# Performance work log

Hardware: AMD Instinct MI355X
Metric: run time of the kernel (lower is better)

Reference implementation:

```python
import jax, jax.numpy as jnp
import numpy as np
from jax import lax

FEAT = 56  # features_size
SR = 2     # sr_ratio
NUM_HEADS = 8

# Constant relative-distance indices, shape (N, N, 2) with values in [0, 2*FEAT-2]
_idx = np.array([[i, j] for i in range(FEAT) for j in range(FEAT)])
REL = jnp.asarray(_idx[None, :, :] - _idx[:, None, :] + FEAT - 1)  # (N, N, 2)


def setup_inputs() -> dict:
    key = jax.random.key(0)
    ks = jax.random.split(key, 8)
    dim = 256
    B = 4
    x = jax.random.normal(ks[0], (B, dim, FEAT, FEAT), dtype=jnp.float32)
    Wq = jax.random.normal(ks[1], (dim, dim), dtype=jnp.float32) * 0.02
    Wkv = jax.random.normal(ks[2], (dim, 2 * dim), dtype=jnp.float32) * 0.02
    sr_w = jax.random.normal(ks[3], (dim, dim, SR, SR), dtype=jnp.float32) * 0.02  # OIHW
    sr_b = jnp.zeros((dim,), dtype=jnp.float32)
    ln_g = jnp.ones((dim,), dtype=jnp.float32)
    ln_b = jnp.zeros((dim,), dtype=jnp.float32)
    pos_emb = jax.random.normal(ks[4], (2 * FEAT - 1, 2 * FEAT - 1), dtype=jnp.float32) * 0.2
    proj_w = jax.random.normal(ks[5], (dim, dim), dtype=jnp.float32) * 0.02
    proj_b = jnp.zeros((dim,), dtype=jnp.float32)
    return {"x": x, "Wq": Wq, "Wkv": Wkv, "sr_w": sr_w, "sr_b": sr_b,
            "ln_g": ln_g, "ln_b": ln_b, "pos_emb": pos_emb,
            "proj_w": proj_w, "proj_b": proj_b}


def reference(x, Wq, Wkv, sr_w, sr_b, ln_g, ln_b, pos_emb, proj_w, proj_b):
    B, C, H, W = x.shape
    N = H * W
    h = NUM_HEADS
    hd = C // h
    scale = hd ** -0.5

    x_q = x.reshape(B, C, N).transpose(0, 2, 1)            # (B, N, C)
    q = (x_q @ Wq).reshape(B, N, h, hd).transpose(0, 2, 1, 3)  # (B, h, N, hd)

    # spatial reduction conv (kernel=stride=SR) + layernorm
    xr = lax.conv_general_dilated(x, sr_w, (SR, SR), 'VALID',
                                  dimension_numbers=('NCHW', 'OIHW', 'NCHW'))
    xr = xr + sr_b[None, :, None, None]
    Nk = (H // SR) * (W // SR)
    x_kv = xr.reshape(B, C, Nk).transpose(0, 2, 1)          # (B, Nk, C)
    mu = jnp.mean(x_kv, axis=-1, keepdims=True)
    var = jnp.var(x_kv, axis=-1, keepdims=True)
    x_kv = (x_kv - mu) * lax.rsqrt(var + 1e-5) * ln_g + ln_b

    # kv projection; einops '(dim h l)' split: head_dim slowest, l fastest
    kv = (x_kv @ Wkv).reshape(B, Nk, hd, h, 2)
    k = kv[..., 0].transpose(0, 3, 1, 2)                    # (B, h, Nk, hd)
    v = kv[..., 1].transpose(0, 3, 1, 2)                    # (B, h, Nk, hd)

    attn = jnp.einsum('bhnd,bhmd->bhnm', q, k) * scale      # (B, h, N, Nk)
    bias = pos_emb[REL[..., 0], REL[..., 1]][:, :Nk]        # (N, Nk)
    attn = jax.nn.softmax(attn + bias, axis=-1)

    out = jnp.einsum('bhnm,bhmd->bhnd', attn, v)            # (B, h, N, hd)
    out = out.transpose(0, 2, 1, 3).reshape(B, N, C)
    out = out @ proj_w + proj_b
    return out.transpose(0, 2, 1).reshape(B, C, H, W)
```

## Files before the change

### kernel.cpp

```cpp
#include <hip/hip_runtime.h>
#include <hip/hip_bf16.h>

typedef float f32x4 __attribute__((ext_vector_type(4)));
typedef short s16x8 __attribute__((ext_vector_type(8)));
typedef unsigned short u16x4 __attribute__((ext_vector_type(4)));
typedef unsigned short u16x8 __attribute__((ext_vector_type(8)));

#define MFMA16(a,b,c) __builtin_amdgcn_mfma_f32_16x16x32_bf16(a,b,c,0,0,0)

#define NTOK 3136
#define NKV  784
#define NKVP 800
#define CD   256
#define NH   8
#define HD   32
#define PEW  111
#define LOG2E 1.4426950408889634f
#define SC2  (0.17677669529663687f * 1.4426950408889634f)

static __device__ __forceinline__ unsigned short f2b(float f){
  unsigned int u = __float_as_uint(f);
  return (unsigned short)((u + 0x7fffu + ((u>>16)&1u)) >> 16);
}
static __device__ __forceinline__ float b2f(unsigned short u){
  return __uint_as_float(((unsigned int)u)<<16);
}
static __device__ __forceinline__ void gload16(const unsigned short* g, unsigned short* l){
  __builtin_amdgcn_global_load_lds(
      (const __attribute__((address_space(1))) unsigned int*)g,
      (__attribute__((address_space(3))) unsigned int*)l, 16, 0, 0);
}
static __device__ __forceinline__ s16x8 pack8(const float* p){
  union { uint4 u; s16x8 s; } w;
  unsigned int a0=__float_as_uint(p[0])+0x8000u, a1=__float_as_uint(p[1])+0x8000u;
  unsigned int a2=__float_as_uint(p[2])+0x8000u, a3=__float_as_uint(p[3])+0x8000u;
  unsigned int a4=__float_as_uint(p[4])+0x8000u, a5=__float_as_uint(p[5])+0x8000u;
  unsigned int a6=__float_as_uint(p[6])+0x8000u, a7=__float_as_uint(p[7])+0x8000u;
  w.u.x = (a0>>16) | (a1 & 0xFFFF0000u);
  w.u.y = (a2>>16) | (a3 & 0xFFFF0000u);
  w.u.z = (a4>>16) | (a5 & 0xFFFF0000u);
  w.u.w = (a6>>16) | (a7 & 0xFFFF0000u);
  return w.s;
}

__global__ __launch_bounds__(256) void k_prep(
      const float* __restrict__ Wq, const float* __restrict__ Wkv,
      const float* __restrict__ pw, const float* __restrict__ srw,
      const float* __restrict__ pos, const float* __restrict__ x,
      unsigned short* __restrict__ WqT, unsigned short* __restrict__ WkvT,
      unsigned short* __restrict__ pwT, unsigned short* __restrict__ srwb2,
      unsigned short* __restrict__ bias2, unsigned short* __restrict__ xbf,
      unsigned short* __restrict__ kb, unsigned short* __restrict__ vT){
  __shared__ float tile[64][65];
  const int blk = blockIdx.x, t = threadIdx.x;
  const int tx = t&15, ty = t>>4;
  if (blk < 64){
    const float* src; unsigned short* dst; int sr0, sc0, sstr;
    if (blk < 16){ src=Wq; dst=WqT; sstr=256; sr0=(blk>>2)*64; sc0=(blk&3)*64; }
    else if (blk < 32){ int b2=blk-16; src=pw; dst=pwT; sstr=256; sr0=(b2>>2)*64; sc0=(b2&3)*64; }
    else { int b2=blk-32; src=Wkv; dst=WkvT; sstr=512; sr0=(b2>>3)*64; sc0=(b2&7)*64; }
#pragma unroll
    for (int j=0;j<4;++j){
      f32x4 v = *(const f32x4*)&src[(size_t)(sr0+ty+j*16)*sstr + sc0 + tx*4];
      tile[ty+j*16][tx*4+0]=v[0]; tile[ty+j*16][tx*4+1]=v[1];
      tile[ty+j*16][tx*4+2]=v[2]; tile[ty+j*16][tx*4+3]=v[3];
    }
    __syncthreads();
    const int nr = t>>2, ccb = (t&3)*16;
    u16x8 o0, o1;
#pragma unroll
    for (int u=0;u<8;++u){ o0[u]=f2b(tile[ccb+u][nr]); o1[u]=f2b(tile[ccb+8+u][nr]); }
    unsigned short* dp = &dst[(size_t)(sc0+nr)*256 + sr0 + ccb];
    *(u16x8*)dp = o0;
    *(u16x8*)(dp+8) = o1;
  } else if (blk < 1088){
    int j = (blk-64)*256 + t;
    int o=j>>10, rem=j&1023, khw=rem>>8, ci=rem&255;
    srwb2[j] = f2b(srw[o*1024 + ci*4 + khw]);
  } else if (blk < 1216){
    int i = (blk-1088)*256 + t;
    if (i < 16384){
      int bh=i>>9, r=i&511, ridx=r>>5, d=r&31;
      int row = 776 + (ridx&7) + (ridx>>3)*16;
      kb[((size_t)bh*NKVP + row)*HD + d] = 0;
    } else {
      int j=i-16384;
      int bh=j>>9, r=j&511, d=r>>4, key=784+(r&15);
      vT[((size_t)bh*HD + d)*NKVP + key] = 0;
    }
  } else if (blk < 4352){
    int n = blk - 1216;
    if (t < 200){
      int nr2 = (n*9363)>>19, nc = n - nr2*56;
      u16x4 o;
#pragma unroll
      for (int j=0;j<4;++j){
        int key = t*4 + j;
        float v;
        if (key < NKV){
          int tt = (key*9363)>>19, mm = key - tt*56;
          v = pos[(tt-nr2+55)*PEW + (mm-nc+55)] * LOG2E;
        } else v = -100000.f;
        o[j] = f2b(v);
      }
      *(u16x4*)&bias2[(size_t)n*NKVP + t*4] = o;
    }
  } else {
    int bx = blk - 4352;
    const int n0 = (bx%49)*64; int c4 = bx/49;
    const int c0 = (c4&3)*64, b = c4>>2;
#pragma unroll
    for (int j=0;j<4;++j){
      f32x4 v = *(const f32x4*)&x[(size_t)(b*CD + c0+ty+j*16)*NTOK + n0 + tx*4];
      tile[ty+j*16][tx*4+0]=v[0]; tile[ty+j*16][tx*4+1]=v[1];
      tile[ty+j*16][tx*4+2]=v[2]; tile[ty+j*16][tx*4+3]=v[3];
    }
    __syncthreads();
    const int nr = t>>2, ccb = (t&3)*16;
    u16x8 o0, o1;
#pragma unroll
    for (int u=0;u<8;++u){ o0[u]=f2b(tile[ccb+u][nr]); o1[u]=f2b(tile[ccb+8+u][nr]); }
    unsigned short* dst = &xbf[((size_t)b*NTOK + n0+nr)*CD + c0 + ccb];
    *(u16x8*)dst = o0;
    *(u16x8*)(dst+8) = o1;
  }
}

__global__ __launch_bounds__(256) void k_qc(const unsigned short* __restrict__ xbf,
      const unsigned short* __restrict__ WqT, const unsigned short* __restrict__ srwb2,
      const float* __restrict__ srb, unsigned short* __restrict__ qb,
      float* __restrict__ convo){
  const int gid = blockIdx.x;
  const int tid=threadIdx.x, wv=tid>>6, l=tid&63, g=l>>4, ln16=l&15;
  if (gid < 784){
    const int bx = gid % 196, by = gid / 196;
    const int bI = bx/49;
    const int n0 = (bx%49)*64;
    const int m0 = n0 + (wv>>1)*32;
    const int c0 = by*64 + (wv&1)*32;
    const unsigned short* ap0 = &xbf[((size_t)bI*NTOK + m0+ln16)*CD + g*8];
    const unsigned short* ap1 = ap0 + 16*CD;
    const unsigned short* bp0 = &WqT[(size_t)(c0+ln16)*CD + g*8];
    const unsigned short* bp1 = bp0 + 16*CD;
    f32x4 acc[2][2] = {};
    s16x8 a0 = *(const s16x8*)ap0, a1 = *(const s16x8*)ap1;
    s16x8 w0 = *(const s16x8*)bp0, w1 = *(const s16x8*)bp1;
#pragma unroll
    for (int k0=0; k0<CD; k0+=32){
      s16x8 na0 = *(const s16x8*)(ap0 + k0+32);
      s16x8 na1 = *(const s16x8*)(ap1 + k0+32);
      s16x8 nw0 = *(const s16x8*)(bp0 + k0+32);
      s16x8 nw1 = *(const s16x8*)(bp1 + k0+32);
      acc[0][0] = MFMA16(a0, w0, acc[0][0]);
      acc[0][1] = MFMA16(a0, w1, acc[0][1]);
      acc[1][0] = MFMA16(a1, w0, acc[1][0]);
      acc[1][1] = MFMA16(a1, w1, acc[1][1]);
      a0=na0; a1=na1; w0=nw0; w1=nw1;
    }
#pragma unroll
    for (int mi=0;mi<2;++mi)
#pragma unroll
      for (int ni=0;ni<2;++ni){
        int c = c0 + ni*16 + ln16;
#pragma unroll
        for (int r=0;r<4;++r){
          int n = m0 + mi*16 + g*4 + r;
          qb[((size_t)bI*NTOK + n)*CD + c] = f2b(acc[mi][ni][r] * SC2);
        }
      }
  } else {
    const int cid = gid - 784;
    const int m0 = (cid%49)*64 + (wv>>1)*32;
    const int c0 = (cid/49)*64 + (wv&1)*32;
    size_t abase[2][4];
#pragma unroll
    for (int mi=0;mi<2;++mi){
      int m = m0 + mi*16 + ln16;
      int bb = (m>=2352)?3:(m>=1568)?2:(m>=784)?1:0;
      int nk = m - bb*784;
      int pp = (nk*9363)>>18, qq = nk - pp*28;
#pragma unroll
      for (int khw=0;khw<4;++khw){
        int kh = khw>>1, kw = khw&1;
        abase[mi][khw] = ((size_t)bb*NTOK + (2*pp+kh)*56 + 2*qq+kw)*CD;
      }
    }
    const unsigned short* wp0 = &srwb2[(size_t)(c0+ln16)*1024 + g*8];
    const unsigned short* wp1 = wp0 + 16*1024;
    f32x4 acc[2][2] = {};
    s16x8 a0 = *(const s16x8*)&xbf[abase[0][0] + g*8];
    s16x8 a1 = *(const s16x8*)&xbf[abase[1][0] + g*8];
    s16x8 w0 = *(const s16x8*)wp0;
    s16x8 w1 = *(const s16x8*)wp1;
#pragma unroll
    for (int s=0; s<32; ++s){
      const int s1 = s+1;
      const int khw2 = (s1>>3)&3, kc2 = (s1&7)*32;
      const int woff = (s1&31)*32;
      s16x8 na0 = *(const s16x8*)&xbf[abase[0][khw2] + kc2 + g*8];
      s16x8 na1 = *(const s16x8*)&xbf[abase[1][khw2] + kc2 + g*8];
      s16x8 nw0 = *(const s16x8*)(wp0 + woff);
      s16x8 nw1 = *(const s16x8*)(wp1 + woff);
      acc[0][0] = MFMA16(a0, w0, acc[0][0]);
      acc[0][1] = MFMA16(a0, w1, acc[0][1]);
      acc[1][0] = MFMA16(a1, w0, acc[1][0]);
      acc[1][1] = MFMA16(a1, w1, acc[1][1]);
      a0=na0; a1=na1; w0=nw0; w1=nw1;
    }
#pragma unroll
    for (int mi=0;mi<2;++mi)
#pragma unroll
      for (int ni=0;ni<2;++ni){
        int c = c0 + ni*16 + ln16;
        float bias = srb[c];
#pragma unroll
        for (int r=0;r<4;++r){
          int m = m0 + mi*16 + g*4 + r;
          convo[(size_t)m*CD + c] = acc[mi][ni][r] + bias;
        }
      }
  }
}

__global__ __launch_bounds__(256) void k_kvln(const float* __restrict__ co,
      const float* __restrict__ gam, const float* __restrict__ bet,
      const unsigned short* __restrict__ WkvT, unsigned short* __restrict__ kb,
      unsigned short* __restrict__ vT){
  __shared__ unsigned short As[64*256];
  const int tid=threadIdx.x, wv=tid>>6, l=tid&63, g=l>>4, ln16=l&15;
  const int m0blk = blockIdx.x*64;
  {
    const int rl = tid>>2, cs = (tid&3)*64;
    const float* src = &co[(size_t)(m0blk+rl)*CD + cs];
    f32x4 vals[16];
    float s=0.f, s2=0.f;
#pragma unroll
    for (int i=0;i<16;++i){
      vals[i] = *(const f32x4*)(src + i*4);
#pragma unroll
      for (int q=0;q<4;++q){ s += vals[i][q]; s2 += vals[i][q]*vals[i][q]; }
    }
    s += __shfl_xor(s,1); s2 += __shfl_xor(s2,1);
    s += __shfl_xor(s,2); s2 += __shfl_xor(s2,2);
    float mu = s*(1.f/CD);
    float rs = rsqrtf(s2*(1.f/CD) - mu*mu + 1e-5f);
#pragma unroll
    for (int u=0;u<8;++u){
      f32x4 g4a = *(const f32x4*)&gam[cs+u*8];
      f32x4 g4b = *(const f32x4*)&gam[cs+u*8+4];
      f32x4 b4a = *(const f32x4*)&bet[cs+u*8];
      f32x4 b4b = *(const f32x4*)&bet[cs+u*8+4];
      u16x8 o;
#pragma unroll
      for (int q=0;q<4;++q){
        o[q]   = f2b((vals[u*2][q]  -mu)*rs*g4a[q] + b4a[q]);
        o[4+q] = f2b((vals[u*2+1][q]-mu)*rs*g4b[q] + b4b[q]);
      }
      int off = (rl*256 + cs + u*8) ^ ((rl&7)<<3);
      *(u16x8*)&As[off] = o;
    }
  }
  __syncthreads();
  const int mw0 = (wv>>1)*32;
  const int c0 = blockIdx.y*64 + (wv&1)*32;
  const unsigned short* bp0 = &WkvT[(size_t)(c0+ln16)*CD + g*8];
  const unsigned short* bp1 = bp0 + 16*CD;
  f32x4 acc[2][2] = {};
  s16x8 w0 = *(const s16x8*)bp0, w1 = *(const s16x8*)bp1;
  const int mr0 = mw0 + ln16, mr1 = mw0 + 16 + ln16;
#pragma unroll
  for (int k0=0; k0<CD; k0+=32){
    s16x8 a0 = *(const s16x8*)&As[(mr0*256 + k0 + g*8) ^ ((mr0&7)<<3)];
    s16x8 a1 = *(const s16x8*)&As[(mr1*256 + k0 + g*8) ^ ((mr1&7)<<3)];
    s16x8 nw0 = w0, nw1 = w1;
    if (k0 < CD-32){
      nw0 = *(const s16x8*)(bp0 + k0+32);
      nw1 = *(const s16x8*)(bp1 + k0+32);
    }
    acc[0][0] = MFMA16(a0, w0, acc[0][0]);
    acc[0][1] = MFMA16(a0, w1, acc[0][1]);
    acc[1][0] = MFMA16(a1, w0, acc[1][0]);
    acc[1][1] = MFMA16(a1, w1, acc[1][1]);
    w0=nw0; w1=nw1;
  }
#pragma unroll
  for (int mi=0;mi<2;++mi)
#pragma unroll
    for (int ni=0;ni<2;++ni){
      int c2 = c0 + ni*16 + ln16;
      int d = c2>>4, hh = (c2>>1)&7;
#pragma unroll
      for (int r=0;r<4;++r){
        int m = m0blk + mw0 + mi*16 + g*4 + r;
        int bq = (m>=2352)?3:(m>=1568)?2:(m>=784)?1:0;
        int nk = m - bq*784;
        unsigned short val = f2b(acc[mi][ni][r]);
        if (c2&1){
          vT[(((size_t)bq*NH+hh)*HD + d)*NKVP + nk] = val;
        } else {
          int chunk = nk & ~31, pos = nk & 31;
          int gg = pos>>3, jj = pos&7;
          int row = (jj<4) ? (gg*4+jj) : (16 + gg*4 + (jj-4));
          kb[(((size_t)bq*NH+hh)*NKVP + chunk + row)*HD + d] = val;
        }
      }
    }
}

__global__ __launch_bounds__(256) void k_attn(const unsigned short* __restrict__ qb,
      const unsigned short* __restrict__ kb, const unsigned short* __restrict__ vT,
      const unsigned short* __restrict__ bias2, unsigned short* __restrict__ aout){
  __shared__ unsigned short kv0[2048], kv1[2048], kv2[2048];
  const int tid=threadIdx.x, wv=tid>>6, l=tid&63, g=l>>4, ln16=l&15;
  const int bh = blockIdx.x, b = bh>>3, h = bh&7;
  const int nq0 = blockIdx.y*128 + wv*16;
  const int nq1 = nq0 + 64;
  const bool act1 = (nq1 < NTOK);
  const int nq1c = act1 ? nq1 : nq0;
  const s16x8 qf0 = *(const s16x8*)&qb[((size_t)b*NTOK + nq0  + ln16)*CD + h*HD + g*8];
  const s16x8 qf1 = *(const s16x8*)&qb[((size_t)b*NTOK + nq1c + ln16)*CD + h*HD + g*8];
  const unsigned short* kbase = kb + (size_t)bh*NKVP*HD;
  const unsigned short* vbase = vT + (size_t)bh*HD*NKVP;
  const unsigned short* bp0 = bias2 + (size_t)(nq0  + ln16)*NKVP + g*8;
  const unsigned short* bp1 = bias2 + (size_t)(nq1c + ln16)*NKVP + g*8;
  const int lslot = ((l&3)^((l>>3)&3))*8;
  const unsigned short* sp = (wv < 2)
      ? (kbase + (size_t)(wv*16 + (l>>2))*HD + lslot)
      : (vbase + (size_t)((wv-2)*16 + (l>>2))*NKVP + lslot);
  const int sstep = (wv < 2) ? 1024 : 32;
  const int ko0 = ln16*32 + (g ^ ((ln16>>1)&3))*8;
  unsigned short *bA = kv0, *bB = kv1, *bC = kv2;
  f32x4 acc00={}, acc01={}, acc10={}, acc11={};
  float S0=0.f, S1=0.f;
  const f32x4 zf = {};
  gload16(sp, bA + wv*512);
  u16x8 bb0 = *(const u16x8*)bp0;
  u16x8 bb1 = *(const u16x8*)bp1;
  gload16(sp + sstep, bB + wv*512);
  u16x8 c0v = *(const u16x8*)(bp0 + 32);
  u16x8 c1v = *(const u16x8*)(bp1 + 32);
  for (int it=0; it<25; ++it){
    if (it < 23) asm volatile("s_waitcnt vmcnt(3)" ::: "memory");
    else         asm volatile("s_waitcnt vmcnt(0)" ::: "memory");
    __builtin_amdgcn_s_barrier();
    __builtin_amdgcn_sched_barrier(0);
    u16x8 n0v = c0v, n1v = c1v;
    if (it < 23){
      gload16(sp + (it+2)*sstep, bC + wv*512);
      n0v = *(const u16x8*)(bp0 + (it+2)*32);
      n1v = *(const u16x8*)(bp1 + (it+2)*32);
    }
    s16x8 ka0 = *(const s16x8*)&bA[ko0];
    s16x8 ka1 = *(const s16x8*)&bA[512 + ko0];
    s16x8 v0  = *(const s16x8*)&bA[1024 + ko0];
    s16x8 v1  = *(const s16x8*)&bA[1536 + ko0];
    __builtin_amdgcn_s_setprio(1);
    f32x4 d00 = MFMA16(ka0, qf0, zf);
    f32x4 d10 = MFMA16(ka1, qf0, zf);
    f32x4 d01 = MFMA16(ka0, qf1, zf);
    f32x4 d11 = MFMA16(ka1, qf1, zf);
    float p0[8], p1[8];
#pragma unroll
    for (int r=0;r<4;++r){
      p0[r]   = exp2f(d00[r] + b2f(bb0[r]));
      p0[4+r] = exp2f(d10[r] + b2f(bb0[4+r]));
      p1[r]   = exp2f(d01[r] + b2f(bb1[r]));
      p1[4+r] = exp2f(d11[r] + b2f(bb1[4+r]));
    }
    S0 += ((p0[0]+p0[1])+(p0[2]+p0[3])) + ((p0[4]+p0[5])+(p0[6]+p0[7]));
    S1 += ((p1[0]+p1[1])+(p1[2]+p1[3])) + ((p1[4]+p1[5])+(p1[6]+p1[7]));
    s16x8 pf0 = pack8(p0);
    s16x8 pf1 = pack8(p1);
    acc00 = MFMA16(pf0, v0, acc00);
    acc01 = MFMA16(pf0, v1, acc01);
    acc10 = MFMA16(pf1, v0, acc10);
    acc11 = MFMA16(pf1, v1, acc11);
    __builtin_amdgcn_s_setprio(0);
    unsigned short* tmp = bA; bA = bB; bB = bC; bC = tmp;
    bb0 = c0v; c0v = n0v;
    bb1 = c1v; c1v = n1v;
  }
  S0 += __shfl_xor(S0, 16); S0 += __shfl_xor(S0, 32);
  S1 += __shfl_xor(S1, 16); S1 += __shfl_xor(S1, 32);
#pragma unroll
  for (int r=0;r<4;++r){
    float inv = 1.f / __shfl(S0, g*4 + r);
    int n = nq0 + g*4 + r;
    aout[((size_t)b*NTOK + n)*CD + h*HD + ln16]      = f2b(acc00[r]*inv);
    aout[((size_t)b*NTOK + n)*CD + h*HD + 16 + ln16] = f2b(acc01[r]*inv);
  }
  if (act1){
#pragma unroll
    for (int r=0;r<4;++r){
      float inv = 1.f / __shfl(S1, g*4 + r);
      int n = nq1 + g*4 + r;
      aout[((size_t)b*NTOK + n)*CD + h*HD + ln16]      = f2b(acc10[r]*inv);
      aout[((size_t)b*NTOK + n)*CD + h*HD + 16 + ln16] = f2b(acc11[r]*inv);
    }
  }
}

__global__ __launch_bounds__(256) void k_proj(const unsigned short* __restrict__ ain,
      const unsigned short* __restrict__ pwT, const float* __restrict__ pb,
      float* __restrict__ out){
  const int tid=threadIdx.x, wv=tid>>6, l=tid&63, g=l>>4, ln16=l&15;
  const int bI = blockIdx.x/49;
  const int n0 = (blockIdx.x%49)*64;
  const int nsub = n0 + (wv&1)*32;
  const int c0 = blockIdx.y*64 + (wv>>1)*32;
  const unsigned short* ap0 = &pwT[(size_t)(c0+ln16)*CD + g*8];
  const unsigned short* ap1 = ap0 + 16*CD;
  const unsigned short* bp0 = &ain[((size_t)bI*NTOK + nsub+ln16)*CD + g*8];
  const unsigned short* bp1 = bp0 + 16*CD;
  f32x4 acc[2][2] = {};
  s16x8 a0 = *(const s16x8*)ap0, a1 = *(const s16x8*)ap1;
  s16x8 w0 = *(const s16x8*)bp0, w1 = *(const s16x8*)bp1;
#pragma unroll
  for (int k0=0; k0<CD; k0+=32){
    s16x8 na0 = *(const s16x8*)(ap0 + k0+32);
    s16x8 na1 = *(const s16x8*)(ap1 + k0+32);
    s16x8 nw0 = *(const s16x8*)(bp0 + k0+32);
    s16x8 nw1 = *(const s16x8*)(bp1 + k0+32);
    acc[0][0] = MFMA16(a0, w0, acc[0][0]);
    acc[0][1] = MFMA16(a0, w1, acc[0][1]);
    acc[1][0] = MFMA16(a1, w0, acc[1][0]);
    acc[1][1] = MFMA16(a1, w1, acc[1][1]);
    a0=na0; a1=na1; w0=nw0; w1=nw1;
  }
#pragma unroll
  for (int mi=0;mi<2;++mi)
#pragma unroll
    for (int r=0;r<4;++r){
      int c = c0 + mi*16 + g*4 + r;
      float bias = pb[c];
#pragma unroll
      for (int ni=0;ni<2;++ni){
        int n = nsub + ni*16 + ln16;
        out[((size_t)bI*CD + c)*NTOK + n] = acc[mi][ni][r] + bias;
      }
    }
}

extern "C" void kernel_launch(void* const* d_in, const int* in_sizes, int n_in,
                              void* d_out, int out_size, void* d_ws, size_t ws_size,
                              hipStream_t stream){
  const float* x   = (const float*)d_in[0];
  const float* Wq  = (const float*)d_in[1];
  const float* Wkv = (const float*)d_in[2];
  const float* srw = (const float*)d_in[3];
  const float* srb = (const float*)d_in[4];
  const float* lng = (const float*)d_in[5];
  const float* lnb = (const float*)d_in[6];
  const float* pos = (const float*)d_in[7];
  const float* pw  = (const float*)d_in[8];
  const float* pb  = (const float*)d_in[9];
  float* out = (float*)d_out;

  unsigned char* p = (unsigned char*)d_ws;
  unsigned short* WqT   = (unsigned short*)(p + 0);
  unsigned short* WkvT  = (unsigned short*)(p + 131072);
  unsigned short* pwT   = (unsigned short*)(p + 393216);
  unsigned short* srwb2 = (unsigned short*)(p + 524288);
  unsigned short* bias2 = (unsigned short*)(p + 1048576);
  unsigned short* xbf   = (unsigned short*)(p + 6066176);
  unsigned short* qbuf  = (unsigned short*)(p + 12488704);
  float*          convo = (float*)        (p + 18911232);
  unsigned short* kbuf  = (unsigned short*)(p + 22122496);
  unsigned short* vT    = (unsigned short*)(p + 23760896);
  unsigned short* aout  = (unsigned short*)(p + 25399296);

  k_prep <<<5136, 256, 0, stream>>>(Wq, Wkv, pw, srw, pos, x,
                                    WqT, WkvT, pwT, srwb2, bias2, xbf, kbuf, vT);
  k_qc   <<<980, 256, 0, stream>>>(xbf, WqT, srwb2, srb, qbuf, convo);
  k_kvln <<<dim3(49,8), 256, 0, stream>>>(convo, lng, lnb, WkvT, kbuf, vT);
  k_attn <<<dim3(32,25), 256, 0, stream>>>(qbuf, kbuf, vT, bias2, aout);
  k_proj <<<dim3(196,4), 256, 0, stream>>>(aout, pwT, pb, out);
}
```

Measured before the change: 200.1 us.

## Deepen GEMM prefetch to two stages and make attention waves independent

The GEMM-style kernels (q, conv, kv, proj) now prefetch operands two k-steps ahead through a three-slot register ring instead of one step ahead. The attention kernel is restructured so each wave owns 16 query rows and its own double-buffered LDS K/V tiles, with no block-wide barriers. The grid doubles from 25 to 49 row blocks to compensate for half the rows per block. This removes barrier stalls and the shared loading split between waves. In exchange, each wave loads its own K/V, so global and LDS traffic rise and register pressure from the deeper prefetch grows.

```diff
diff --git a/kernel.cpp b/kernel.cpp
--- a/kernel.cpp
+++ b/kernel.cpp
@@ -143,19 +143,24 @@
     const unsigned short* bp0 = &WqT[(size_t)(c0+ln16)*CD + g*8];
     const unsigned short* bp1 = bp0 + 16*CD;
     f32x4 acc[2][2] = {};
-    s16x8 a0 = *(const s16x8*)ap0, a1 = *(const s16x8*)ap1;
-    s16x8 w0 = *(const s16x8*)bp0, w1 = *(const s16x8*)bp1;
-#pragma unroll
-    for (int k0=0; k0<CD; k0+=32){
-      s16x8 na0 = *(const s16x8*)(ap0 + k0+32);
-      s16x8 na1 = *(const s16x8*)(ap1 + k0+32);
-      s16x8 nw0 = *(const s16x8*)(bp0 + k0+32);
-      s16x8 nw1 = *(const s16x8*)(bp1 + k0+32);
-      acc[0][0] = MFMA16(a0, w0, acc[0][0]);
-      acc[0][1] = MFMA16(a0, w1, acc[0][1]);
-      acc[1][0] = MFMA16(a1, w0, acc[1][0]);
-      acc[1][1] = MFMA16(a1, w1, acc[1][1]);
-      a0=na0; a1=na1; w0=nw0; w1=nw1;
+    s16x8 ra0[3], ra1[3], rw0[3], rw1[3];
+    ra0[0]=*(const s16x8*)ap0; ra1[0]=*(const s16x8*)ap1;
+    rw0[0]=*(const s16x8*)bp0; rw1[0]=*(const s16x8*)bp1;
+    ra0[1]=*(const s16x8*)(ap0+32); ra1[1]=*(const s16x8*)(ap1+32);
+    rw0[1]=*(const s16x8*)(bp0+32); rw1[1]=*(const s16x8*)(bp1+32);
+#pragma unroll
+    for (int i=0;i<8;++i){
+      if (i<6){
+        ra0[(i+2)%3]=*(const s16x8*)(ap0+(i+2)*32);
+        ra1[(i+2)%3]=*(const s16x8*)(ap1+(i+2)*32);
+        rw0[(i+2)%3]=*(const s16x8*)(bp0+(i+2)*32);
+        rw1[(i+2)%3]=*(const s16x8*)(bp1+(i+2)*32);
+      }
+      const int c = i%3;
+      acc[0][0] = MFMA16(ra0[c], rw0[c], acc[0][0]);
+      acc[0][1] = MFMA16(ra0[c], rw1[c], acc[0][1]);
+      acc[1][0] = MFMA16(ra1[c], rw0[c], acc[1][0]);
+      acc[1][1] = MFMA16(ra1[c], rw1[c], acc[1][1]);
     }
 #pragma unroll
     for (int mi=0;mi<2;++mi)
@@ -188,24 +193,29 @@
     const unsigned short* wp0 = &srwb2[(size_t)(c0+ln16)*1024 + g*8];
     const unsigned short* wp1 = wp0 + 16*1024;
     f32x4 acc[2][2] = {};
-    s16x8 a0 = *(const s16x8*)&xbf[abase[0][0] + g*8];
-    s16x8 a1 = *(const s16x8*)&xbf[abase[1][0] + g*8];
-    s16x8 w0 = *(const s16x8*)wp0;
-    s16x8 w1 = *(const s16x8*)wp1;
+    s16x8 ra0[3], ra1[3], rw0[3], rw1[3];
+    ra0[0]=*(const s16x8*)&xbf[abase[0][0] + g*8];
+    ra1[0]=*(const s16x8*)&xbf[abase[1][0] + g*8];
+    rw0[0]=*(const s16x8*)wp0; rw1[0]=*(const s16x8*)wp1;
+    ra0[1]=*(const s16x8*)&xbf[abase[0][0] + 32 + g*8];
+    ra1[1]=*(const s16x8*)&xbf[abase[1][0] + 32 + g*8];
+    rw0[1]=*(const s16x8*)(wp0+32); rw1[1]=*(const s16x8*)(wp1+32);
 #pragma unroll
     for (int s=0; s<32; ++s){
-      const int s1 = s+1;
-      const int khw2 = (s1>>3)&3, kc2 = (s1&7)*32;
-      const int woff = (s1&31)*32;
-      s16x8 na0 = *(const s16x8*)&xbf[abase[0][khw2] + kc2 + g*8];
-      s16x8 na1 = *(const s16x8*)&xbf[abase[1][khw2] + kc2 + g*8];
-      s16x8 nw0 = *(const s16x8*)(wp0 + woff);
-      s16x8 nw1 = *(const s16x8*)(wp1 + woff);
-      acc[0][0] = MFMA16(a0, w0, acc[0][0]);
-      acc[0][1] = MFMA16(a0, w1, acc[0][1]);
-      acc[1][0] = MFMA16(a1, w0, acc[1][0]);
-      acc[1][1] = MFMA16(a1, w1, acc[1][1]);
-      a0=na0; a1=na1; w0=nw0; w1=nw1;
+      if (s<30){
+        const int s2 = s+2;
+        const int khw2 = (s2>>3)&3, kc2 = (s2&7)*32;
+        const int woff = s2*32;
+        ra0[s2%3]=*(const s16x8*)&xbf[abase[0][khw2] + kc2 + g*8];
+        ra1[s2%3]=*(const s16x8*)&xbf[abase[1][khw2] + kc2 + g*8];
+        rw0[s2%3]=*(const s16x8*)(wp0 + woff);
+        rw1[s2%3]=*(const s16x8*)(wp1 + woff);
+      }
+      const int c = s%3;
+      acc[0][0] = MFMA16(ra0[c], rw0[c], acc[0][0]);
+      acc[0][1] = MFMA16(ra0[c], rw1[c], acc[0][1]);
+      acc[1][0] = MFMA16(ra1[c], rw0[c], acc[1][0]);
+      acc[1][1] = MFMA16(ra1[c], rw1[c], acc[1][1]);
     }
 #pragma unroll
     for (int mi=0;mi<2;++mi)
@@ -266,22 +276,24 @@
   const unsigned short* bp0 = &WkvT[(size_t)(c0+ln16)*CD + g*8];
   const unsigned short* bp1 = bp0 + 16*CD;
   f32x4 acc[2][2] = {};
-  s16x8 w0 = *(const s16x8*)bp0, w1 = *(const s16x8*)bp1;
+  s16x8 rw0[3], rw1[3];
+  rw0[0]=*(const s16x8*)bp0; rw1[0]=*(const s16x8*)bp1;
+  rw0[1]=*(const s16x8*)(bp0+32); rw1[1]=*(const s16x8*)(bp1+32);
   const int mr0 = mw0 + ln16, mr1 = mw0 + 16 + ln16;
 #pragma unroll
-  for (int k0=0; k0<CD; k0+=32){
+  for (int i=0;i<8;++i){
+    if (i<6){
+      rw0[(i+2)%3]=*(const s16x8*)(bp0+(i+2)*32);
+      rw1[(i+2)%3]=*(const s16x8*)(bp1+(i+2)*32);
+    }
+    const int k0 = i*32;
     s16x8 a0 = *(const s16x8*)&As[(mr0*256 + k0 + g*8) ^ ((mr0&7)<<3)];
     s16x8 a1 = *(const s16x8*)&As[(mr1*256 + k0 + g*8) ^ ((mr1&7)<<3)];
-    s16x8 nw0 = w0, nw1 = w1;
-    if (k0 < CD-32){
-      nw0 = *(const s16x8*)(bp0 + k0+32);
-      nw1 = *(const s16x8*)(bp1 + k0+32);
-    }
-    acc[0][0] = MFMA16(a0, w0, acc[0][0]);
-    acc[0][1] = MFMA16(a0, w1, acc[0][1]);
-    acc[1][0] = MFMA16(a1, w0, acc[1][0]);
-    acc[1][1] = MFMA16(a1, w1, acc[1][1]);
-    w0=nw0; w1=nw1;
+    const int c = i%3;
+    acc[0][0] = MFMA16(a0, rw0[c], acc[0][0]);
+    acc[0][1] = MFMA16(a0, rw1[c], acc[0][1]);
+    acc[1][0] = MFMA16(a1, rw0[c], acc[1][0]);
+    acc[1][1] = MFMA16(a1, rw1[c], acc[1][1]);
   }
 #pragma unroll
   for (int mi=0;mi<2;++mi)
@@ -310,93 +322,73 @@
 __global__ __launch_bounds__(256) void k_attn(const unsigned short* __restrict__ qb,
       const unsigned short* __restrict__ kb, const unsigned short* __restrict__ vT,
       const unsigned short* __restrict__ bias2, unsigned short* __restrict__ aout){
-  __shared__ unsigned short kv0[2048], kv1[2048], kv2[2048];
+  __shared__ unsigned short kvb[4][2][2048];
   const int tid=threadIdx.x, wv=tid>>6, l=tid&63, g=l>>4, ln16=l&15;
   const int bh = blockIdx.x, b = bh>>3, h = bh&7;
-  const int nq0 = blockIdx.y*128 + wv*16;
-  const int nq1 = nq0 + 64;
-  const bool act1 = (nq1 < NTOK);
-  const int nq1c = act1 ? nq1 : nq0;
-  const s16x8 qf0 = *(const s16x8*)&qb[((size_t)b*NTOK + nq0  + ln16)*CD + h*HD + g*8];
-  const s16x8 qf1 = *(const s16x8*)&qb[((size_t)b*NTOK + nq1c + ln16)*CD + h*HD + g*8];
-  const unsigned short* kbase = kb + (size_t)bh*NKVP*HD;
-  const unsigned short* vbase = vT + (size_t)bh*HD*NKVP;
-  const unsigned short* bp0 = bias2 + (size_t)(nq0  + ln16)*NKVP + g*8;
-  const unsigned short* bp1 = bias2 + (size_t)(nq1c + ln16)*NKVP + g*8;
-  const int lslot = ((l&3)^((l>>3)&3))*8;
-  const unsigned short* sp = (wv < 2)
-      ? (kbase + (size_t)(wv*16 + (l>>2))*HD + lslot)
-      : (vbase + (size_t)((wv-2)*16 + (l>>2))*NKVP + lslot);
-  const int sstep = (wv < 2) ? 1024 : 32;
+  const int nw = blockIdx.y*64 + wv*16;
+  const s16x8 qf = *(const s16x8*)&qb[((size_t)b*NTOK + nw + ln16)*CD + h*HD + g*8];
+  const int r4 = l>>2;
+  const int sg = ((l&3) ^ ((r4>>1)&3))*8;
+  const unsigned short* kp = kb + (size_t)bh*NKVP*HD + (size_t)r4*HD + sg;
+  const unsigned short* vp = vT + (size_t)bh*HD*NKVP + (size_t)r4*NKVP + sg;
+  const unsigned short* bp = bias2 + (size_t)(nw + ln16)*NKVP + g*8;
+  unsigned short* my0 = &kvb[wv][0][0];
+  unsigned short* my1 = &kvb[wv][1][0];
   const int ko0 = ln16*32 + (g ^ ((ln16>>1)&3))*8;
-  unsigned short *bA = kv0, *bB = kv1, *bC = kv2;
-  f32x4 acc00={}, acc01={}, acc10={}, acc11={};
-  float S0=0.f, S1=0.f;
+  f32x4 accO0 = {}, accO1 = {};
+  float S = 0.f;
   const f32x4 zf = {};
-  gload16(sp, bA + wv*512);
-  u16x8 bb0 = *(const u16x8*)bp0;
-  u16x8 bb1 = *(const u16x8*)bp1;
-  gload16(sp + sstep, bB + wv*512);
-  u16x8 c0v = *(const u16x8*)(bp0 + 32);
-  u16x8 c1v = *(const u16x8*)(bp1 + 32);
+  gload16(kp,        my0);
+  gload16(kp+512,    my0+512);
+  gload16(vp,        my0+1024);
+  gload16(vp+16*NKVP, my0+1536);
+  u16x8 bb = *(const u16x8*)bp;
+  kp += 1024; vp += 32; bp += 32;
+#pragma unroll 2
   for (int it=0; it<25; ++it){
-    if (it < 23) asm volatile("s_waitcnt vmcnt(3)" ::: "memory");
-    else         asm volatile("s_waitcnt vmcnt(0)" ::: "memory");
-    __builtin_amdgcn_s_barrier();
-    __builtin_amdgcn_sched_barrier(0);
-    u16x8 n0v = c0v, n1v = c1v;
-    if (it < 23){
-      gload16(sp + (it+2)*sstep, bC + wv*512);
-      n0v = *(const u16x8*)(bp0 + (it+2)*32);
-      n1v = *(const u16x8*)(bp1 + (it+2)*32);
-    }
-    s16x8 ka0 = *(const s16x8*)&bA[ko0];
-    s16x8 ka1 = *(const s16x8*)&bA[512 + ko0];
-    s16x8 v0  = *(const s16x8*)&bA[1024 + ko0];
-    s16x8 v1  = *(const s16x8*)&bA[1536 + ko0];
+    unsigned short* cur = (it&1) ? my1 : my0;
+    unsigned short* nxt = (it&1) ? my0 : my1;
+    u16x8 nbb = bb;
+    if (it < 24){
+      gload16(kp,         nxt);
+      gload16(kp+512,     nxt+512);
+      gload16(vp,         nxt+1024);
+      gload16(vp+16*NKVP, nxt+1536);
+      nbb = *(const u16x8*)bp;
+      kp += 1024; vp += 32; bp += 32;
+      asm volatile("s_waitcnt vmcnt(5)" ::: "memory");
+    } else {
+      asm volatile("s_waitcnt vmcnt(0)" ::: "memory");
+    }
+    s16x8 ka0 = *(const s16x8*)&cur[ko0];
+    s16x8 ka1 = *(const s16x8*)&cur[512 + ko0];
+    s16x8 v0  = *(const s16x8*)&cur[1024 + ko0];
+    s16x8 v1  = *(const s16x8*)&cur[1536 + ko0];
     __builtin_amdgcn_s_setprio(1);
-    f32x4 d00 = MFMA16(ka0, qf0, zf);
-    f32x4 d10 = MFMA16(ka1, qf0, zf);
-    f32x4 d01 = MFMA16(ka0, qf1, zf);
-    f32x4 d11 = MFMA16(ka1, qf1, zf);
-    float p0[8], p1[8];
+    f32x4 d0 = MFMA16(ka0, qf, zf);
+    f32x4 d1 = MFMA16(ka1, qf, zf);
+    float p[8];
 #pragma unroll
     for (int r=0;r<4;++r){
-      p0[r]   = exp2f(d00[r] + b2f(bb0[r]));
-      p0[4+r] = exp2f(d10[r] + b2f(bb0[4+r]));
-      p1[r]   = exp2f(d01[r] + b2f(bb1[r]));
-      p1[4+r] = exp2f(d11[r] + b2f(bb1[4+r]));
-    }
-    S0 += ((p0[0]+p0[1])+(p0[2]+p0[3])) + ((p0[4]+p0[5])+(p0[6]+p0[7]));
-    S1 += ((p1[0]+p1[1])+(p1[2]+p1[3])) + ((p1[4]+p1[5])+(p1[6]+p1[7]));
-    s16x8 pf0 = pack8(p0);
-    s16x8 pf1 = pack8(p1);
-    acc00 = MFMA16(pf0, v0, acc00);
-    acc01 = MFMA16(pf0, v1, acc01);
-    acc10 = MFMA16(pf1, v0, acc10);
-    acc11 = MFMA16(pf1, v1, acc11);
+      p[r]   = exp2f(d0[r] + b2f(bb[r]));
+      p[4+r] = exp2f(d1[r] + b2f(bb[4+r]));
+    }
+    S += ((p[0]+p[1])+(p[2]+p[3])) + ((p[4]+p[5])+(p[6]+p[7]));
+    s16x8 pf = pack8(p);
+    accO0 = MFMA16(pf, v0, accO0);
+    accO1 = MFMA16(pf, v1, accO1);
     __builtin_amdgcn_s_setprio(0);
-    unsigned short* tmp = bA; bA = bB; bB = bC; bC = tmp;
-    bb0 = c0v; c0v = n0v;
-    bb1 = c1v; c1v = n1v;
-  }
-  S0 += __shfl_xor(S0, 16); S0 += __shfl_xor(S0, 32);
-  S1 += __shfl_xor(S1, 16); S1 += __shfl_xor(S1, 32);
+    bb = nbb;
+  }
+  S += __shfl_xor(S, 16);
+  S += __shfl_xor(S, 32);
 #pragma unroll
   for (int r=0;r<4;++r){
-    float inv = 1.f / __shfl(S0, g*4 + r);
-    int n = nq0 + g*4 + r;
-    aout[((size_t)b*NTOK + n)*CD + h*HD + ln16]      = f2b(acc00[r]*inv);
-    aout[((size_t)b*NTOK + n)*CD + h*HD + 16 + ln16] = f2b(acc01[r]*inv);
-  }
-  if (act1){
-#pragma unroll
-    for (int r=0;r<4;++r){
-      float inv = 1.f / __shfl(S1, g*4 + r);
-      int n = nq1 + g*4 + r;
-      aout[((size_t)b*NTOK + n)*CD + h*HD + ln16]      = f2b(acc10[r]*inv);
-      aout[((size_t)b*NTOK + n)*CD + h*HD + 16 + ln16] = f2b(acc11[r]*inv);
-    }
+    float Sr = __shfl(S, g*4 + r);
+    float inv = 1.f / Sr;
+    int n = nw + g*4 + r;
+    aout[((size_t)b*NTOK + n)*CD + h*HD + ln16]      = f2b(accO0[r]*inv);
+    aout[((size_t)b*NTOK + n)*CD + h*HD + 16 + ln16] = f2b(accO1[r]*inv);
   }
 }
 
@@ -413,19 +405,24 @@
   const unsigned short* bp0 = &ain[((size_t)bI*NTOK + nsub+ln16)*CD + g*8];
   const unsigned short* bp1 = bp0 + 16*CD;
   f32x4 acc[2][2] = {};
-  s16x8 a0 = *(const s16x8*)ap0, a1 = *(const s16x8*)ap1;
-  s16x8 w0 = *(const s16x8*)bp0, w1 = *(const s16x8*)bp1;
-#pragma unroll
-  for (int k0=0; k0<CD; k0+=32){
-    s16x8 na0 = *(const s16x8*)(ap0 + k0+32);
-    s16x8 na1 = *(const s16x8*)(ap1 + k0+32);
-    s16x8 nw0 = *(const s16x8*)(bp0 + k0+32);
-    s16x8 nw1 = *(const s16x8*)(bp1 + k0+32);
-    acc[0][0] = MFMA16(a0, w0, acc[0][0]);
-    acc[0][1] = MFMA16(a0, w1, acc[0][1]);
-    acc[1][0] = MFMA16(a1, w0, acc[1][0]);
-    acc[1][1] = MFMA16(a1, w1, acc[1][1]);
-    a0=na0; a1=na1; w0=nw0; w1=nw1;
+  s16x8 ra0[3], ra1[3], rw0[3], rw1[3];
+  ra0[0]=*(const s16x8*)ap0; ra1[0]=*(const s16x8*)ap1;
+  rw0[0]=*(const s16x8*)bp0; rw1[0]=*(const s16x8*)bp1;
+  ra0[1]=*(const s16x8*)(ap0+32); ra1[1]=*(const s16x8*)(ap1+32);
+  rw0[1]=*(const s16x8*)(bp0+32); rw1[1]=*(const s16x8*)(bp1+32);
+#pragma unroll
+  for (int i=0;i<8;++i){
+    if (i<6){
+      ra0[(i+2)%3]=*(const s16x8*)(ap0+(i+2)*32);
+      ra1[(i+2)%3]=*(const s16x8*)(ap1+(i+2)*32);
+      rw0[(i+2)%3]=*(const s16x8*)(bp0+(i+2)*32);
+      rw1[(i+2)%3]=*(const s16x8*)(bp1+(i+2)*32);
+    }
+    const int c = i%3;
+    acc[0][0] = MFMA16(ra0[c], rw0[c], acc[0][0]);
+    acc[0][1] = MFMA16(ra0[c], rw1[c], acc[0][1]);
+    acc[1][0] = MFMA16(ra1[c], rw0[c], acc[1][0]);
+    acc[1][1] = MFMA16(ra1[c], rw1[c], acc[1][1]);
   }
 #pragma unroll
   for (int mi=0;mi<2;++mi)
@@ -473,6 +470,6 @@
                                     WqT, WkvT, pwT, srwb2, bias2, xbf, kbuf, vT);
   k_qc   <<<980, 256, 0, stream>>>(xbf, WqT, srwb2, srb, qbuf, convo);
   k_kvln <<<dim3(49,8), 256, 0, stream>>>(convo, lng, lnb, WkvT, kbuf, vT);
-  k_attn <<<dim3(32,25), 256, 0, stream>>>(qbuf, kbuf, vT, bias2, aout);
+  k_attn <<<dim3(32,49), 256, 0, stream>>>(qbuf, kbuf, vT, bias2, aout);
   k_proj <<<dim3(196,4), 256, 0, stream>>>(aout, pwT, pb, out);
 }
```

Measured after the change: 206.6 us. 3.3% more time.
